# Optimization experiments

Hardware: AMD Instinct MI355X
Metric: run time of the kernel (lower is better)

Reference implementation:

```python
import jax, jax.numpy as jnp
import numpy as np

B = 1024
IN_FEATURES = 4096
OUT_FEATURES = 4096
TOP_K = 64  # both k_prev (input width) and output top_k in this config


def setup_inputs() -> dict:
    key = jax.random.key(0)
    k1, k2, k3, k4 = jax.random.split(key, 4)
    bound = 1.0 / np.sqrt(IN_FEATURES)
    return {
        "input": jax.random.normal(k1, (B, TOP_K), dtype=jnp.float32),
        "weight": jax.random.uniform(k2, (OUT_FEATURES, IN_FEATURES), dtype=jnp.float32, minval=-bound, maxval=bound),
        "bias": jax.random.uniform(k3, (OUT_FEATURES,), dtype=jnp.float32, minval=-bound, maxval=bound),
        "previously_selected_nodes": jax.random.randint(k4, (B, TOP_K), 0, IN_FEATURES, dtype=jnp.int64).astype(jnp.int32),
    }


def reference(input, weight, bias, previously_selected_nodes):
    # Gather selected input-dim columns of weight per sample:
    # weight: (O, I), idx: (B, K) -> w_sel: (B, K, O)
    w_sel = jnp.take(weight.T, previously_selected_nodes, axis=0)
    # Batched matvec: (B, K, O) x (B, K) -> (B, O), plus bias
    result = jnp.einsum("bko,bk->bo", w_sel, input) + bias
    # Top-k selection over out_features, keep values and indices
    values, selected_nodes = jax.lax.top_k(result, TOP_K)
    return values, selected_nodes
```

## Files before the change

### kernel.cpp

```cpp
#include <hip/hip_runtime.h>
#include <stdint.h>

#define B_N 1024
#define K_N 64
#define O_N 4096
#define I_N 4096

typedef float nvec4 __attribute__((ext_vector_type(4)));

__global__ __launch_bounds__(256) void xpose_small(
    const float* __restrict__ x, const float* __restrict__ idxf,
    float* __restrict__ xT, float* __restrict__ idxTf) {
  __shared__ float tile[64][65];
  const int t = threadIdx.x;
  const int which = blockIdx.x >> 4;
  const int b0 = (blockIdx.x & 15) * 64;
  const float* src = which ? idxf : x;
  float* dst = which ? idxTf : xT;
  {
    const int r = t & 63;
    const int q0 = t >> 6;
#pragma unroll
    for (int jj = 0; jj < 4; ++jj) {
      const int q = q0 + 4 * jj;
      const float4 v = *(const float4*)(src + (size_t)(b0 + r) * K_N + 4 * q);
      tile[r][4 * q + 0] = v.x;
      tile[r][4 * q + 1] = v.y;
      tile[r][4 * q + 2] = v.z;
      tile[r][4 * q + 3] = v.w;
    }
  }
  __syncthreads();
  {
    const int kk = t & 63;
    const int q0 = t >> 6;
#pragma unroll
    for (int jj = 0; jj < 4; ++jj) {
      const int qb = q0 + 4 * jj;
      float4 v;
      v.x = tile[4 * qb + 0][kk];
      v.y = tile[4 * qb + 1][kk];
      v.z = tile[4 * qb + 2][kk];
      v.w = tile[4 * qb + 3][kk];
      *(float4*)(dst + (size_t)kk * B_N + b0 + 4 * qb) = v;
    }
  }
}

__global__ __launch_bounds__(1024, 4) void gemv_lds(
    const float* __restrict__ W, const float* __restrict__ xT,
    const int* __restrict__ idxT, const float* __restrict__ bias,
    float* __restrict__ res) {
  __shared__ float4 Wi[I_N];
  const int t = threadIdx.x;
  const int o0 = blockIdx.x * 4;

  {
    const int i0 = 4 * t;
    const nvec4 r0 = __builtin_nontemporal_load(
        (const nvec4*)(W + (size_t)(o0 + 0) * I_N + i0));
    const nvec4 r1 = __builtin_nontemporal_load(
        (const nvec4*)(W + (size_t)(o0 + 1) * I_N + i0));
    const nvec4 r2 = __builtin_nontemporal_load(
        (const nvec4*)(W + (size_t)(o0 + 2) * I_N + i0));
    const nvec4 r3 = __builtin_nontemporal_load(
        (const nvec4*)(W + (size_t)(o0 + 3) * I_N + i0));
    Wi[i0 + 0] = make_float4(r0.x, r1.x, r2.x, r3.x);
    Wi[i0 + 1] = make_float4(r0.y, r1.y, r2.y, r3.y);
    Wi[i0 + 2] = make_float4(r0.z, r1.z, r2.z, r3.z);
    Wi[i0 + 3] = make_float4(r0.w, r1.w, r2.w, r3.w);
  }
  __syncthreads();

  const int b = t;
  const float4 bv = *(const float4*)(bias + o0);
  float4 a = make_float4(0.f, 0.f, 0.f, 0.f);
  float xr[4];
  int ir[4];
#pragma unroll
  for (int d = 0; d < 4; ++d) {
    xr[d] = xT[d * B_N + b];
    ir[d] = idxT[d * B_N + b];
  }
#pragma unroll
  for (int k = 0; k < K_N; ++k) {
    const float xk = xr[k & 3];
    const int i = ir[k & 3];
    if (k + 4 < K_N) {
      xr[k & 3] = xT[(k + 4) * B_N + b];
      ir[k & 3] = idxT[(k + 4) * B_N + b];
    }
    const float4 w = Wi[i];
    a.x = __fadd_rn(a.x, __fmul_rn(xk, w.x));
    a.y = __fadd_rn(a.y, __fmul_rn(xk, w.y));
    a.z = __fadd_rn(a.z, __fmul_rn(xk, w.z));
    a.w = __fadd_rn(a.w, __fmul_rn(xk, w.w));
  }
  a.x = __fadd_rn(a.x, bv.x);
  a.y = __fadd_rn(a.y, bv.y);
  a.z = __fadd_rn(a.z, bv.z);
  a.w = __fadd_rn(a.w, bv.w);
  *(float4*)(res + (size_t)b * O_N + o0) = a;
}

__global__ __launch_bounds__(256) void topk_phase(
    const float* __restrict__ res, float* __restrict__ out) {
  __shared__ __align__(16) unsigned int hist[256];
  __shared__ unsigned int hist4[4 * 257];
  __shared__ unsigned int sel_u[64];
  __shared__ int sel_i[64];
  __shared__ int eqlist[128];
  __shared__ unsigned int s_cntgt, s_cnteq;
  __shared__ unsigned int s_remaining, s_prefix;

  const int t = threadIdx.x;
  const int b = blockIdx.x;
  const int w = t >> 6;

  hist[t] = 0u;
#pragma unroll
  for (int j = 0; j < 5; ++j) {
    const int z = t + 256 * j;
    if (z < 4 * 257) hist4[z] = 0u;
  }
  if (t == 0) {
    s_remaining = 64u;
    s_prefix = 0u;
    s_cntgt = 0u;
    s_cnteq = 0u;
  }

  unsigned int myu[16];
#pragma unroll
  for (int jf = 0; jf < 4; ++jf) {
    const float4 v =
        *(const float4*)(res + (size_t)b * O_N + 1024 * jf + 4 * t);
    const float fv[4] = {v.x, v.y, v.z, v.w};
#pragma unroll
    for (int c = 0; c < 4; ++c) {
      const unsigned int s = __float_as_uint(fv[c]);
      myu[jf * 4 + c] = (s & 0x80000000u) ? ~s : (s | 0x80000000u);
    }
  }
  __syncthreads();

  for (int round = 3; round >= 0; --round) {
    const int shift = round * 8;
    const unsigned int pfx = s_prefix;
    const unsigned int rem = s_remaining;
    if (round == 3) {
#pragma unroll
      for (int j = 0; j < 16; ++j)
        atomicAdd(&hist4[w * 257 + (myu[j] >> 24)], 1u);
    } else {
      const unsigned int himask = 0xFFFFFFFFu << (shift + 8);
#pragma unroll
      for (int j = 0; j < 16; ++j) {
        if ((myu[j] & himask) == (pfx & himask))
          atomicAdd(&hist[(myu[j] >> shift) & 255u], 1u);
      }
    }
    __syncthreads();
    if (t < 64) {
      uint4 h;
      if (round == 3) {
        h.x = hist4[0 * 257 + 4 * t + 0] + hist4[1 * 257 + 4 * t + 0] +
              hist4[2 * 257 + 4 * t + 0] + hist4[3 * 257 + 4 * t + 0];
        h.y = hist4[0 * 257 + 4 * t + 1] + hist4[1 * 257 + 4 * t + 1] +
              hist4[2 * 257 + 4 * t + 1] + hist4[3 * 257 + 4 * t + 1];
        h.z = hist4[0 * 257 + 4 * t + 2] + hist4[1 * 257 + 4 * t + 2] +
              hist4[2 * 257 + 4 * t + 2] + hist4[3 * 257 + 4 * t + 2];
        h.w = hist4[0 * 257 + 4 * t + 3] + hist4[1 * 257 + 4 * t + 3] +
              hist4[2 * 257 + 4 * t + 3] + hist4[3 * 257 + 4 * t + 3];
      } else {
        h = *(const uint4*)&hist[4 * t];
      }
      unsigned int s0 = h.x + h.y + h.z + h.w;
      unsigned int run = s0;
#pragma unroll
      for (int off = 1; off < 64; off <<= 1) {
        const unsigned int v = __shfl_down(run, off, 64);
        if (t + off < 64) run += v;
      }
      const unsigned int above = run - s0;
      unsigned int cge[4], cgt[4];
      cgt[3] = above;
      cge[3] = above + h.w;
      cgt[2] = cge[3];
      cge[2] = cge[3] + h.z;
      cgt[1] = cge[2];
      cge[1] = cge[2] + h.y;
      cgt[0] = cge[1];
      cge[0] = cge[1] + h.x;
#pragma unroll
      for (int j = 0; j < 4; ++j) {
        if (cge[j] >= rem && cgt[j] < rem) {
          s_prefix = pfx | ((unsigned int)(4 * t + j) << shift);
          s_remaining = rem - cgt[j];
        }
      }
      *(uint4*)&hist[4 * t] = make_uint4(0u, 0u, 0u, 0u);
    }
    __syncthreads();
  }
  const unsigned int ustar = s_prefix;

#pragma unroll
  for (int j = 0; j < 16; ++j) {
    const unsigned int u = myu[j];
    const int oi = 4 * t + (j & 3) + 1024 * (j >> 2);
    if (u > ustar) {
      unsigned int p = atomicAdd(&s_cntgt, 1u);
      sel_u[p] = u;
      sel_i[p] = oi;
    } else if (u == ustar) {
      unsigned int p = atomicAdd(&s_cnteq, 1u);
      if (p < 128u) eqlist[p] = oi;
    }
  }
  __syncthreads();

  if (t == 0 && s_cnteq > 1u) {
    int n = (int)(s_cnteq < 128u ? s_cnteq : 128u);
    for (int a = 1; a < n; ++a) {
      int v = eqlist[a];
      int c = a;
      while (c > 0 && eqlist[c - 1] > v) {
        eqlist[c] = eqlist[c - 1];
        --c;
      }
      eqlist[c] = v;
    }
  }
  __syncthreads();

  if (t < 64) {
    const int n_gt = (int)s_cntgt;
    unsigned int u;
    int oi;
    if (t < n_gt) {
      u = sel_u[t];
      oi = sel_i[t];
    } else {
      u = ustar;
      oi = eqlist[t - n_gt];
    }
    unsigned long long key =
        ((unsigned long long)(~u) << 32) | (unsigned int)oi;
    for (int kk = 2; kk <= 64; kk <<= 1) {
      for (int jj = kk >> 1; jj > 0; jj >>= 1) {
        unsigned long long partner = __shfl_xor(key, jj, 64);
        const bool up = ((t & kk) == 0);
        const bool lower = ((t & jj) == 0);
        unsigned long long mn = key < partner ? key : partner;
        unsigned long long mx = key < partner ? partner : key;
        key = (up == lower) ? mn : mx;
      }
    }
    const unsigned int su = ~(unsigned int)(key >> 32);
    const int so = (int)(key & 0xFFFFFFFFu);
    const float f = (su & 0x80000000u) ? __uint_as_float(su ^ 0x80000000u)
                                       : __uint_as_float(~su);
    out[b * 64 + t] = f;
    out[B_N * 64 + b * 64 + t] = (float)so;
  }
}

__global__ __launch_bounds__(256) void selgemv_topk(
    const float* __restrict__ x, const float* __restrict__ Wsrc,
    const float* __restrict__ bias, const int* __restrict__ idx,
    float* __restrict__ out) {
  __shared__ float sx[K_N];
  __shared__ int si[K_N];
  __shared__ float svals[O_N];
  __shared__ unsigned int hist[256];
  __shared__ unsigned int scan[256];
  __shared__ unsigned int sel_u[64];
  __shared__ int sel_i[64];
  __shared__ int eqlist[128];
  __shared__ unsigned int s_T, s_ngt, s_cntgt, s_cnteq;
  __shared__ unsigned int s_remaining, s_prefix;

  const int t = threadIdx.x;
  const int b = blockIdx.x;

  if (t < K_N) {
    sx[t] = x[b * K_N + t];
    si[t] = idx[b * K_N + t];
  }
  if (t == 0) {
    s_remaining = 64u;
    s_prefix = 0u;
    s_cntgt = 0u;
    s_cnteq = 0u;
  }
  __syncthreads();

  float acc[16];
#pragma unroll
  for (int j = 0; j < 16; ++j) acc[j] = 0.0f;

  for (int k = 0; k < K_N; ++k) {
    const float xk = sx[k];
    const int ik = si[k];
#pragma unroll
    for (int j = 0; j < 4; ++j) {
      int o0 = (j * 256 + t) * 4;
#pragma unroll
      for (int c = 0; c < 4; ++c) {
        float w = Wsrc[(size_t)(o0 + c) * I_N + ik];
        acc[4 * j + c] = __fadd_rn(acc[4 * j + c], __fmul_rn(xk, w));
      }
    }
  }

#pragma unroll
  for (int j = 0; j < 4; ++j) {
    int g = j * 256 + t;
    float4 bb = ((const float4*)bias)[g];
    float4 r;
    r.x = __fadd_rn(acc[4 * j + 0], bb.x);
    r.y = __fadd_rn(acc[4 * j + 1], bb.y);
    r.z = __fadd_rn(acc[4 * j + 2], bb.z);
    r.w = __fadd_rn(acc[4 * j + 3], bb.w);
    ((float4*)svals)[g] = r;
  }
  __syncthreads();

  unsigned int myu[16];
#pragma unroll
  for (int j = 0; j < 16; ++j) {
    float f = svals[t + 256 * j];
    unsigned int s = __float_as_uint(f);
    myu[j] = (s & 0x80000000u) ? ~s : (s | 0x80000000u);
  }

  for (int round = 3; round >= 0; --round) {
    const int shift = round * 8;
    hist[t] = 0u;
    __syncthreads();
    const unsigned int pfx = s_prefix;
    const unsigned int rem = s_remaining;
    const unsigned int himask =
        (round == 3) ? 0u : (0xFFFFFFFFu << (shift + 8));
#pragma unroll
    for (int j = 0; j < 16; ++j) {
      if ((myu[j] & himask) == (pfx & himask))
        atomicAdd(&hist[(myu[j] >> shift) & 255u], 1u);
    }
    __syncthreads();
    scan[t] = hist[t];
    __syncthreads();
    for (int off = 1; off < 256; off <<= 1) {
      unsigned int v = (t + off < 256) ? scan[t + off] : 0u;
      __syncthreads();
      scan[t] += v;
      __syncthreads();
    }
    const unsigned int c_ge = scan[t];
    const unsigned int c_gt = (t < 255) ? scan[t + 1] : 0u;
    if (c_ge >= rem && c_gt < rem) {
      s_T = (unsigned int)t;
      s_ngt = c_gt;
    }
    __syncthreads();
    if (t == 0) {
      s_prefix |= (s_T << shift);
      s_remaining -= s_ngt;
    }
    __syncthreads();
  }
  const unsigned int ustar = s_prefix;

#pragma unroll
  for (int j = 0; j < 16; ++j) {
    const unsigned int u = myu[j];
    if (u > ustar) {
      unsigned int p = atomicAdd(&s_cntgt, 1u);
      sel_u[p] = u;
      sel_i[p] = t + 256 * j;
    } else if (u == ustar) {
      unsigned int p = atomicAdd(&s_cnteq, 1u);
      if (p < 128u) eqlist[p] = t + 256 * j;
    }
  }
  __syncthreads();

  if (t == 0 && s_cnteq > 1u) {
    int n = (int)(s_cnteq < 128u ? s_cnteq : 128u);
    for (int a = 1; a < n; ++a) {
      int v = eqlist[a];
      int c = a;
      while (c > 0 && eqlist[c - 1] > v) {
        eqlist[c] = eqlist[c - 1];
        --c;
      }
      eqlist[c] = v;
    }
  }
  __syncthreads();

  if (t < 64) {
    const int n_gt = (int)s_cntgt;
    unsigned int u;
    int oi;
    if (t < n_gt) {
      u = sel_u[t];
      oi = sel_i[t];
    } else {
      u = ustar;
      oi = eqlist[t - n_gt];
    }
    unsigned long long key =
        ((unsigned long long)(~u) << 32) | (unsigned int)oi;
    for (int kk = 2; kk <= 64; kk <<= 1) {
      for (int jj = kk >> 1; jj > 0; jj >>= 1) {
        unsigned long long partner = __shfl_xor(key, jj, 64);
        const bool up = ((t & kk) == 0);
        const bool lower = ((t & jj) == 0);
        unsigned long long mn = key < partner ? key : partner;
        unsigned long long mx = key < partner ? partner : key;
        key = (up == lower) ? mn : mx;
      }
    }
    const unsigned int su = ~(unsigned int)(key >> 32);
    const int so = (int)(key & 0xFFFFFFFFu);
    const float f = (su & 0x80000000u) ? __uint_as_float(su ^ 0x80000000u)
                                       : __uint_as_float(~su);
    out[b * 64 + t] = f;
    out[B_N * 64 + b * 64 + t] = (float)so;
  }
}

extern "C" void kernel_launch(void* const* d_in, const int* in_sizes, int n_in,
                              void* d_out, int out_size, void* d_ws,
                              size_t ws_size, hipStream_t stream) {
  const float* x = (const float*)d_in[0];
  const float* W = (const float*)d_in[1];
  const float* bias = (const float*)d_in[2];
  const int* idx = (const int*)d_in[3];
  float* out = (float*)d_out;

  const size_t xT_bytes = (size_t)K_N * B_N * sizeof(float);
  const size_t idxT_bytes = xT_bytes;
  const size_t res_bytes = (size_t)B_N * O_N * sizeof(float);

  if (ws_size >= xT_bytes + idxT_bytes + res_bytes) {
    float* xT = (float*)d_ws;
    float* idxTf = (float*)((char*)d_ws + xT_bytes);
    float* res = (float*)((char*)d_ws + xT_bytes + idxT_bytes);
    xpose_small<<<32, 256, 0, stream>>>(x, (const float*)idx, xT, idxTf);
    gemv_lds<<<O_N / 4, 1024, 0, stream>>>(W, xT, (const int*)idxTf, bias,
                                           res);
    topk_phase<<<B_N, 256, 0, stream>>>(res, out);
  } else {
    selgemv_topk<<<B_N, 256, 0, stream>>>(x, W, bias, idx, out);
  }
}
```

Baseline: 156.8 us.

## Process 16 output columns per block with prefetched second weight tile

```diff
diff --git a/kernel.cpp b/kernel.cpp
--- a/kernel.cpp
+++ b/kernel.cpp
@@ -47,60 +47,108 @@
   }
 }
 
-__global__ __launch_bounds__(1024, 4) void gemv_lds(
+#define GEMV_COMPUTE(G)                                                   \
+  do {                                                                    \
+    const int o0 = (G)*8;                                                 \
+    const int b = t;                                                      \
+    const float4 bvA = *(const float4*)(bias + o0);                       \
+    const float4 bvB = *(const float4*)(bias + o0 + 4);                   \
+    float4 aA = make_float4(0.f, 0.f, 0.f, 0.f);                          \
+    float4 aB = make_float4(0.f, 0.f, 0.f, 0.f);                          \
+    float xr[4];                                                          \
+    int ir[4];                                                            \
+    _Pragma("unroll") for (int d = 0; d < 4; ++d) {                       \
+      xr[d] = xT[d * B_N + b];                                            \
+      ir[d] = idxT[d * B_N + b];                                          \
+    }                                                                     \
+    _Pragma("unroll") for (int k = 0; k < K_N; ++k) {                     \
+      const float xk = xr[k & 3];                                         \
+      const int i = ir[k & 3];                                            \
+      if (k + 4 < K_N) {                                                  \
+        xr[k & 3] = xT[(k + 4) * B_N + b];                                \
+        ir[k & 3] = idxT[(k + 4) * B_N + b];                              \
+      }                                                                   \
+      const float4 wA = Wi[i];                                            \
+      const float4 wB = Wi[I_N + i];                                      \
+      aA.x = __fadd_rn(aA.x, __fmul_rn(xk, wA.x));                        \
+      aA.y = __fadd_rn(aA.y, __fmul_rn(xk, wA.y));                        \
+      aA.z = __fadd_rn(aA.z, __fmul_rn(xk, wA.z));                        \
+      aA.w = __fadd_rn(aA.w, __fmul_rn(xk, wA.w));                        \
+      aB.x = __fadd_rn(aB.x, __fmul_rn(xk, wB.x));                        \
+      aB.y = __fadd_rn(aB.y, __fmul_rn(xk, wB.y));                        \
+      aB.z = __fadd_rn(aB.z, __fmul_rn(xk, wB.z));                        \
+      aB.w = __fadd_rn(aB.w, __fmul_rn(xk, wB.w));                        \
+    }                                                                     \
+    aA.x = __fadd_rn(aA.x, bvA.x);                                        \
+    aA.y = __fadd_rn(aA.y, bvA.y);                                        \
+    aA.z = __fadd_rn(aA.z, bvA.z);                                        \
+    aA.w = __fadd_rn(aA.w, bvA.w);                                        \
+    aB.x = __fadd_rn(aB.x, bvB.x);                                        \
+    aB.y = __fadd_rn(aB.y, bvB.y);                                        \
+    aB.z = __fadd_rn(aB.z, bvB.z);                                        \
+    aB.w = __fadd_rn(aB.w, bvB.w);                                        \
+    *(float4*)(res + (size_t)b * O_N + o0) = aA;                          \
+    *(float4*)(res + (size_t)b * O_N + o0 + 4) = aB;                      \
+  } while (0)
+
+__global__ __launch_bounds__(1024, 4) void gemv_lds8(
     const float* __restrict__ W, const float* __restrict__ xT,
     const int* __restrict__ idxT, const float* __restrict__ bias,
     float* __restrict__ res) {
-  __shared__ float4 Wi[I_N];
+  __shared__ float4 Wi[2 * I_N];
   const int t = threadIdx.x;
-  const int o0 = blockIdx.x * 4;
-
+  const int i0 = 4 * t;
+  const int xcd = blockIdx.x & 7;
+  const int jj = blockIdx.x >> 3;
+  const int g0 = (xcd * 32 + jj) * 2;
+
+  nvec4 r0, r1, r2, r3, r4, r5, r6, r7;
   {
-    const int i0 = 4 * t;
-    const nvec4 r0 = __builtin_nontemporal_load(
-        (const nvec4*)(W + (size_t)(o0 + 0) * I_N + i0));
-    const nvec4 r1 = __builtin_nontemporal_load(
-        (const nvec4*)(W + (size_t)(o0 + 1) * I_N + i0));
-    const nvec4 r2 = __builtin_nontemporal_load(
-        (const nvec4*)(W + (size_t)(o0 + 2) * I_N + i0));
-    const nvec4 r3 = __builtin_nontemporal_load(
-        (const nvec4*)(W + (size_t)(o0 + 3) * I_N + i0));
-    Wi[i0 + 0] = make_float4(r0.x, r1.x, r2.x, r3.x);
-    Wi[i0 + 1] = make_float4(r0.y, r1.y, r2.y, r3.y);
-    Wi[i0 + 2] = make_float4(r0.z, r1.z, r2.z, r3.z);
-    Wi[i0 + 3] = make_float4(r0.w, r1.w, r2.w, r3.w);
-  }
-  __syncthreads();
-
-  const int b = t;
-  const float4 bv = *(const float4*)(bias + o0);
-  float4 a = make_float4(0.f, 0.f, 0.f, 0.f);
-  float xr[4];
-  int ir[4];
-#pragma unroll
-  for (int d = 0; d < 4; ++d) {
-    xr[d] = xT[d * B_N + b];
-    ir[d] = idxT[d * B_N + b];
-  }
-#pragma unroll
-  for (int k = 0; k < K_N; ++k) {
-    const float xk = xr[k & 3];
-    const int i = ir[k & 3];
-    if (k + 4 < K_N) {
-      xr[k & 3] = xT[(k + 4) * B_N + b];
-      ir[k & 3] = idxT[(k + 4) * B_N + b];
-    }
-    const float4 w = Wi[i];
-    a.x = __fadd_rn(a.x, __fmul_rn(xk, w.x));
-    a.y = __fadd_rn(a.y, __fmul_rn(xk, w.y));
-    a.z = __fadd_rn(a.z, __fmul_rn(xk, w.z));
-    a.w = __fadd_rn(a.w, __fmul_rn(xk, w.w));
-  }
-  a.x = __fadd_rn(a.x, bv.x);
-  a.y = __fadd_rn(a.y, bv.y);
-  a.z = __fadd_rn(a.z, bv.z);
-  a.w = __fadd_rn(a.w, bv.w);
-  *(float4*)(res + (size_t)b * O_N + o0) = a;
+    const float* Wp = W + (size_t)g0 * 8 * I_N + i0;
+    r0 = __builtin_nontemporal_load((const nvec4*)(Wp + 0 * (size_t)I_N));
+    r1 = __builtin_nontemporal_load((const nvec4*)(Wp + 1 * (size_t)I_N));
+    r2 = __builtin_nontemporal_load((const nvec4*)(Wp + 2 * (size_t)I_N));
+    r3 = __builtin_nontemporal_load((const nvec4*)(Wp + 3 * (size_t)I_N));
+    r4 = __builtin_nontemporal_load((const nvec4*)(Wp + 4 * (size_t)I_N));
+    r5 = __builtin_nontemporal_load((const nvec4*)(Wp + 5 * (size_t)I_N));
+    r6 = __builtin_nontemporal_load((const nvec4*)(Wp + 6 * (size_t)I_N));
+    r7 = __builtin_nontemporal_load((const nvec4*)(Wp + 7 * (size_t)I_N));
+  }
+  Wi[i0 + 0] = make_float4(r0.x, r1.x, r2.x, r3.x);
+  Wi[i0 + 1] = make_float4(r0.y, r1.y, r2.y, r3.y);
+  Wi[i0 + 2] = make_float4(r0.z, r1.z, r2.z, r3.z);
+  Wi[i0 + 3] = make_float4(r0.w, r1.w, r2.w, r3.w);
+  Wi[I_N + i0 + 0] = make_float4(r4.x, r5.x, r6.x, r7.x);
+  Wi[I_N + i0 + 1] = make_float4(r4.y, r5.y, r6.y, r7.y);
+  Wi[I_N + i0 + 2] = make_float4(r4.z, r5.z, r6.z, r7.z);
+  Wi[I_N + i0 + 3] = make_float4(r4.w, r5.w, r6.w, r7.w);
+  {
+    const float* Wp = W + ((size_t)g0 + 1) * 8 * I_N + i0;
+    r0 = __builtin_nontemporal_load((const nvec4*)(Wp + 0 * (size_t)I_N));
+    r1 = __builtin_nontemporal_load((const nvec4*)(Wp + 1 * (size_t)I_N));
+    r2 = __builtin_nontemporal_load((const nvec4*)(Wp + 2 * (size_t)I_N));
+    r3 = __builtin_nontemporal_load((const nvec4*)(Wp + 3 * (size_t)I_N));
+    r4 = __builtin_nontemporal_load((const nvec4*)(Wp + 4 * (size_t)I_N));
+    r5 = __builtin_nontemporal_load((const nvec4*)(Wp + 5 * (size_t)I_N));
+    r6 = __builtin_nontemporal_load((const nvec4*)(Wp + 6 * (size_t)I_N));
+    r7 = __builtin_nontemporal_load((const nvec4*)(Wp + 7 * (size_t)I_N));
+  }
+  __syncthreads();
+
+  GEMV_COMPUTE(g0);
+
+  __syncthreads();
+  Wi[i0 + 0] = make_float4(r0.x, r1.x, r2.x, r3.x);
+  Wi[i0 + 1] = make_float4(r0.y, r1.y, r2.y, r3.y);
+  Wi[i0 + 2] = make_float4(r0.z, r1.z, r2.z, r3.z);
+  Wi[i0 + 3] = make_float4(r0.w, r1.w, r2.w, r3.w);
+  Wi[I_N + i0 + 0] = make_float4(r4.x, r5.x, r6.x, r7.x);
+  Wi[I_N + i0 + 1] = make_float4(r4.y, r5.y, r6.y, r7.y);
+  Wi[I_N + i0 + 2] = make_float4(r4.z, r5.z, r6.z, r7.z);
+  Wi[I_N + i0 + 3] = make_float4(r4.w, r5.w, r6.w, r7.w);
+  __syncthreads();
+
+  GEMV_COMPUTE(g0 + 1);
 }
 
 __global__ __launch_bounds__(256) void topk_phase(
@@ -450,8 +498,7 @@
     float* idxTf = (float*)((char*)d_ws + xT_bytes);
     float* res = (float*)((char*)d_ws + xT_bytes + idxT_bytes);
     xpose_small<<<32, 256, 0, stream>>>(x, (const float*)idx, xT, idxTf);
-    gemv_lds<<<O_N / 4, 1024, 0, stream>>>(W, xT, (const int*)idxTf, bias,
-                                           res);
+    gemv_lds8<<<256, 1024, 0, stream>>>(W, xT, (const int*)idxTf, bias, res);
     topk_phase<<<B_N, 256, 0, stream>>>(res, out);
   } else {
     selgemv_topk<<<B_N, 256, 0, stream>>>(x, W, bias, idx, out);
```

Measured after the change: 152.2 us. -2.9%, faster.
